# Optimization experiments

Hardware: AMD Instinct MI355X
Metric: run time of the kernel (lower is better)

## Reference

```python
import jax, jax.numpy as jnp
import numpy as np

N = 50000   # nodes
E = 800000  # edges
V = 10000   # vocab
D = 128     # emb_dim
H = 128     # hidden_dim
C = 10      # num_classes
G = 512     # graphs in batch


def setup_inputs() -> dict:
    key = jax.random.key(0)
    ks = jax.random.split(key, 10)
    return {
        "x_tokens": jax.random.randint(ks[0], (N,), 0, V),
        "edge_index": jax.random.randint(ks[1], (2, E), 0, N),
        "batch": jnp.sort(jax.random.randint(ks[2], (N,), 0, G)),
        "emb": jax.random.normal(ks[3], (V, D), dtype=jnp.float32) * 0.05,
        "w1": jax.random.normal(ks[4], (D, H), dtype=jnp.float32) * 0.05,
        "b1": jax.random.normal(ks[5], (H,), dtype=jnp.float32) * 0.05,
        "w2": jax.random.normal(ks[6], (H, H), dtype=jnp.float32) * 0.05,
        "b2": jax.random.normal(ks[7], (H,), dtype=jnp.float32) * 0.05,
        "lin_w": jax.random.normal(ks[8], (H, C), dtype=jnp.float32) * 0.05,
        "lin_b": jax.random.normal(ks[9], (C,), dtype=jnp.float32) * 0.05,
    }


def _gcn_conv(x, W, b, src, dst, norm):
    # PyG GCNConv: x' = D^{-1/2}(A+I)D^{-1/2} X W + b (self-loops already in src/dst)
    h = x @ W                                  # [N, H]
    msg = h[src] * norm[:, None]               # [E+N, H] gather + scale
    return jax.ops.segment_sum(msg, dst, num_segments=N) + b


def reference(x_tokens, edge_index, batch, emb, w1, b1, w2, b2, lin_w, lin_b):
    # embedding with padding_idx=0 (row 0 forced to zero)
    table = emb * (jnp.arange(V) != 0)[:, None].astype(emb.dtype)
    x = table[x_tokens]                        # [N, D]

    # add self loops, symmetric degree normalization (computed once)
    loops = jnp.arange(N)
    src = jnp.concatenate([edge_index[0], loops])
    dst = jnp.concatenate([edge_index[1], loops])
    deg = jax.ops.segment_sum(jnp.ones_like(dst, dtype=x.dtype), dst, num_segments=N)
    dis = jax.lax.rsqrt(deg)                   # deg >= 1 due to self loops
    norm = dis[src] * dis[dst]                 # [E+N]

    x = jax.nn.relu(_gcn_conv(x, w1, b1, src, dst, norm))
    x = jax.nn.relu(_gcn_conv(x, w2, b2, src, dst, norm))

    # global mean pool over graphs
    sums = jax.ops.segment_sum(x, batch, num_segments=G)          # [G, H]
    cnts = jax.ops.segment_sum(jnp.ones((N,), x.dtype), batch, num_segments=G)
    pooled = sums / jnp.maximum(cnts, 1.0)[:, None]

    return pooled @ lin_w + lin_b              # [G, C]
```

## Files before the change

### kernel.cpp

```cpp
#include <hip/hip_runtime.h>
#include <hip/hip_bf16.h>


typedef unsigned int uint;
typedef unsigned short ushort;
typedef __attribute__((ext_vector_type(8))) short bf16x8;
typedef __attribute__((ext_vector_type(4))) float f32x4;

__device__ inline float bf_lo(uint u) { return __uint_as_float(u << 16); }
__device__ inline float bf_hi(uint u) { return __uint_as_float(u & 0xffff0000u); }
__device__ inline ushort f2bf(float f) {
    uint u = __float_as_uint(f);
    return (ushort)((u + 0x7fffu + ((u >> 16) & 1u)) >> 16);
}
__device__ inline uint pack2bf(float a, float b) {
    return (uint)f2bf(a) | ((uint)f2bf(b) << 16);
}

#define EPB 2048
#define CAP 8192

__global__ __launch_bounds__(256) void init_convert(int4* __restrict__ z, int n4,
                                                    const float* __restrict__ W1,
                                                    const float* __restrict__ W2,
                                                    ushort* __restrict__ W1t,
                                                    ushort* __restrict__ W2t) {
    const int zb = (n4 + 255) >> 8;
    if ((int)blockIdx.x < zb) {
        int i = blockIdx.x * 256 + threadIdx.x;
        if (i < n4) z[i] = make_int4(0, 0, 0, 0);
    } else {
        int i = (blockIdx.x - zb) * 256 + threadIdx.x;
        const float* Ws = (i < 16384) ? W1 : W2;
        ushort* Wd      = (i < 16384) ? W1t : W2t;
        int j = i & 16383;
        int nn = j >> 7, k = j & 127;
        Wd[j] = f2bf(Ws[k * 128 + nn]);
    }
}

__global__ __launch_bounds__(256) void bucket_scatter(const int* __restrict__ src,
                                                      const int* __restrict__ dst,
                                                      int* __restrict__ bcur,
                                                      uint* __restrict__ bstage,
                                                      int E, int NB) {
    __shared__ int lh[256];
    __shared__ int lbase[257];
    __shared__ int gbase[256];
    __shared__ int lcur[256];
    __shared__ uint stage[EPB];
    const int t = threadIdx.x;
    const int base = blockIdx.x * EPB;
    const int end  = min(E, base + EPB);
    const int tot  = end - base;

    lh[t] = 0;
    __syncthreads();

    uint pk[8]; int bk[8]; int cnt = 0;
    for (int i = base + t; i < end; i += 256) {
        int s = src[i];
        uint d = (uint)dst[i];
        bk[cnt] = (int)(d >> 8);
        pk[cnt] = (uint)s | ((d & 255u) << 24);
        atomicAdd(&lh[bk[cnt]], 1);
        ++cnt;
    }
    __syncthreads();

    if (t < NB && lh[t]) gbase[t] = t * CAP + atomicAdd(&bcur[t], lh[t]);
    {
        __shared__ int ls[256];
        int v = lh[t];
        ls[t] = v;
        __syncthreads();
        for (int off = 1; off < 256; off <<= 1) {
            int x = (t >= off) ? ls[t - off] : 0;
            __syncthreads();
            ls[t] += x;
            __syncthreads();
        }
        lbase[t] = ls[t] - v;
        if (t == 255) lbase[256] = ls[255];
        lcur[t] = 0;
    }
    __syncthreads();

    for (int j = 0; j < cnt; ++j) {
        int p = lbase[bk[j]] + atomicAdd(&lcur[bk[j]], 1);
        stage[p] = pk[j];
    }
    __syncthreads();

    for (int i = t; i < tot; i += 256) {
        int lo = 0, hi = 256;
        while (lo + 1 < hi) {
            int mid = (lo + hi) >> 1;
            if (lbase[mid] <= i) lo = mid; else hi = mid;
        }
        bstage[gbase[lo] + (i - lbase[lo])] = stage[i];
    }
}

__global__ __launch_bounds__(256) void csr_build(const uint* __restrict__ bstage,
                                                 const int* __restrict__ bcur,
                                                 float* __restrict__ dis,
                                                 int* __restrict__ rbeg,
                                                 int* __restrict__ rend,
                                                 int* __restrict__ csr,
                                                 int N, int NB) {
    __shared__ int lh[256];
    __shared__ int ls[256];
    __shared__ int lbase[256];
    __shared__ int lcur[256];
    const int b = blockIdx.x;
    const int t = threadIdx.x;
    const int base  = b * CAP;
    const int cntb  = bcur[b];
    const int n0    = b << 8;
    const int nn    = min(256, N - n0);

    lh[t] = 0;
    __syncthreads();
    for (int i = t; i < cntb; i += 256)
        atomicAdd(&lh[bstage[base + i] >> 24], 1);
    __syncthreads();

    const int v = lh[t];
    ls[t] = v;
    __syncthreads();
    for (int off = 1; off < 256; off <<= 1) {
        int x = (t >= off) ? ls[t - off] : 0;
        __syncthreads();
        ls[t] += x;
        __syncthreads();
    }
    lbase[t] = ls[t] - v;
    lcur[t] = 0;
    if (t < nn) {
        dis[n0 + t]  = rsqrtf((float)v + 1.0f);
        rbeg[n0 + t] = base + lbase[t];
        rend[n0 + t] = base + lbase[t] + v;
    }
    __syncthreads();

    for (int i = t; i < cntb; i += 256) {
        uint e = bstage[base + i];
        int dl = (int)(e >> 24);
        int pos = base + lbase[dl] + atomicAdd(&lcur[dl], 1);
        csr[pos] = (int)(e & 0xFFFFFFu);
    }
}

template<bool GATHER>
__global__ __launch_bounds__(256) void gemm_mfma(const ushort* __restrict__ Xbf,
                                                 const int* __restrict__ tokens,
                                                 const float* __restrict__ emb,
                                                 const ushort* __restrict__ Wt,
                                                 const float* __restrict__ dis,
                                                 ushort* __restrict__ Out, int n) {
    __shared__ ushort wl[128 * 128];
    const int tid = threadIdx.x;

    {
        const int row  = tid >> 1;
        const int half = tid & 1;
        const int base = row * 256 + half * 128;
#pragma unroll
        for (int i = 0; i < 8; ++i) {
            int off = base + i * 16;
            uint4 v = *(const uint4*)((const char*)Wt + off);
            int swz = off ^ ((row & 7) << 4);
            *(uint4*)((char*)wl + swz) = v;
        }
    }
    __syncthreads();

    const int w  = tid >> 6;
    const int l  = tid & 63;
    const int lr = l & 15;
    const int lg = l >> 4;
    const int rowBase = blockIdx.x * 128 + w * 32;

    f32x4 acc[2][8];
#pragma unroll
    for (int s = 0; s < 2; ++s)
#pragma unroll
        for (int ct = 0; ct < 8; ++ct) acc[s][ct] = (f32x4){0.f, 0.f, 0.f, 0.f};

    bf16x8 afrag[2][4];
#pragma unroll
    for (int s = 0; s < 2; ++s) {
        const int row = rowBase + s * 16 + lr;
        if (row < n) {
            if (GATHER) {
                const int tok = tokens[row];
                if (tok != 0) {
                    const float* ep = emb + (size_t)tok * 128;
#pragma unroll
                    for (int kk = 0; kk < 4; ++kk) {
                        const float* q = ep + kk * 32 + lg * 8;
                        float4 lo = *(const float4*)q;
                        float4 hi = *(const float4*)(q + 4);
                        uint4 pk;
                        pk.x = pack2bf(lo.x, lo.y); pk.y = pack2bf(lo.z, lo.w);
                        pk.z = pack2bf(hi.x, hi.y); pk.w = pack2bf(hi.z, hi.w);
                        union { uint4 u; bf16x8 b; } c; c.u = pk;
                        afrag[s][kk] = c.b;
                    }
                } else {
#pragma unroll
                    for (int kk = 0; kk < 4; ++kk) afrag[s][kk] = (bf16x8){0,0,0,0,0,0,0,0};
                }
            } else {
                const ushort* xp = Xbf + (size_t)row * 128;
#pragma unroll
                for (int kk = 0; kk < 4; ++kk)
                    afrag[s][kk] = *(const bf16x8*)(xp + kk * 32 + lg * 8);
            }
        } else {
#pragma unroll
            for (int kk = 0; kk < 4; ++kk) afrag[s][kk] = (bf16x8){0,0,0,0,0,0,0,0};
        }
    }

#pragma unroll
    for (int ct = 0; ct < 8; ++ct) {
#pragma unroll
        for (int kk = 0; kk < 4; ++kk) {
            const int nrow = ct * 16 + lr;
            int off = nrow * 256 + kk * 64 + lg * 16;
            off ^= ((nrow & 7) << 4);
            bf16x8 b = *(const bf16x8*)((const char*)wl + off);
            acc[0][ct] = __builtin_amdgcn_mfma_f32_16x16x32_bf16(afrag[0][kk], b, acc[0][ct], 0, 0, 0);
            acc[1][ct] = __builtin_amdgcn_mfma_f32_16x16x32_bf16(afrag[1][kk], b, acc[1][ct], 0, 0, 0);
        }
    }

#pragma unroll
    for (int s = 0; s < 2; ++s) {
#pragma unroll
        for (int r = 0; r < 4; ++r) {
            const int row = rowBase + s * 16 + lg * 4 + r;
            if (row < n) {
                const float sc = dis[row];
                ushort* op = Out + (size_t)row * 128 + lr;
#pragma unroll
                for (int ct = 0; ct < 8; ++ct)
                    op[ct * 16] = f2bf(acc[s][ct][r] * sc);
            }
        }
    }
}

template<bool FUSE_POOL>
__global__ __launch_bounds__(256) void aggregate_kernel(const ushort* __restrict__ H,
                                                        const float* __restrict__ dis,
                                                        const int* __restrict__ rbeg,
                                                        const int* __restrict__ rend,
                                                        const int* __restrict__ csr,
                                                        const float* __restrict__ bias,
                                                        ushort* __restrict__ Out,
                                                        const int* __restrict__ batch,
                                                        float* __restrict__ pooled,
                                                        int n) {
    const int g = threadIdx.x >> 4;
    const int l = threadIdx.x & 15;
    const int node = blockIdx.x * 16 + g;
    const bool valid = node < n;

    float s0_=0.f,s1_=0.f,s2_=0.f,s3_=0.f,s4_=0.f,s5_=0.f,s6_=0.f,s7_=0.f;
    float dn = 0.f;
    const float4 bA = *(const float4*)&bias[l * 8];
    const float4 bB = *(const float4*)&bias[l * 8 + 4];

    if (valid) {
        dn = dis[node];
        const uint4 hq = *(const uint4*)(H + (size_t)node * 128 + l * 8);
        s0_ = bf_lo(hq.x); s1_ = bf_hi(hq.x);
        s2_ = bf_lo(hq.y); s3_ = bf_hi(hq.y);
        s4_ = bf_lo(hq.z); s5_ = bf_hi(hq.z);
        s6_ = bf_lo(hq.w); s7_ = bf_hi(hq.w);

        const int e0 = rbeg[node];
        const int e1 = rend[node];
        int e = e0;
        for (; e + 8 <= e1; e += 8) {
            int a[8];
#pragma unroll
            for (int j = 0; j < 8; ++j) a[j] = csr[e + j];
            uint4 h[8];
#pragma unroll
            for (int j = 0; j < 8; ++j) h[j] = *(const uint4*)(H + (size_t)a[j] * 128 + l * 8);
#pragma unroll
            for (int j = 0; j < 8; ++j) {
                s0_ += bf_lo(h[j].x); s1_ += bf_hi(h[j].x);
                s2_ += bf_lo(h[j].y); s3_ += bf_hi(h[j].y);
                s4_ += bf_lo(h[j].z); s5_ += bf_hi(h[j].z);
                s6_ += bf_lo(h[j].w); s7_ += bf_hi(h[j].w);
            }
        }
        for (; e + 4 <= e1; e += 4) {
            int a[4];
#pragma unroll
            for (int j = 0; j < 4; ++j) a[j] = csr[e + j];
            uint4 h[4];
#pragma unroll
            for (int j = 0; j < 4; ++j) h[j] = *(const uint4*)(H + (size_t)a[j] * 128 + l * 8);
#pragma unroll
            for (int j = 0; j < 4; ++j) {
                s0_ += bf_lo(h[j].x); s1_ += bf_hi(h[j].x);
                s2_ += bf_lo(h[j].y); s3_ += bf_hi(h[j].y);
                s4_ += bf_lo(h[j].z); s5_ += bf_hi(h[j].z);
                s6_ += bf_lo(h[j].w); s7_ += bf_hi(h[j].w);
            }
        }
        for (; e < e1; ++e) {
            const uint4 h = *(const uint4*)(H + (size_t)csr[e] * 128 + l * 8);
            s0_ += bf_lo(h.x); s1_ += bf_hi(h.x);
            s2_ += bf_lo(h.y); s3_ += bf_hi(h.y);
            s4_ += bf_lo(h.z); s5_ += bf_hi(h.z);
            s6_ += bf_lo(h.w); s7_ += bf_hi(h.w);
        }
    }

    const float o0 = fmaxf(s0_ * dn + bA.x, 0.0f);
    const float o1 = fmaxf(s1_ * dn + bA.y, 0.0f);
    const float o2 = fmaxf(s2_ * dn + bA.z, 0.0f);
    const float o3 = fmaxf(s3_ * dn + bA.w, 0.0f);
    const float o4 = fmaxf(s4_ * dn + bB.x, 0.0f);
    const float o5 = fmaxf(s5_ * dn + bB.y, 0.0f);
    const float o6 = fmaxf(s6_ * dn + bB.z, 0.0f);
    const float o7 = fmaxf(s7_ * dn + bB.w, 0.0f);

    if constexpr (!FUSE_POOL) {
        if (valid) {
            uint4 o;
            o.x = pack2bf(o0, o1); o.y = pack2bf(o2, o3);
            o.z = pack2bf(o4, o5); o.w = pack2bf(o6, o7);
            *(uint4*)(Out + (size_t)node * 128 + l * 8) = o;
        }
    } else {
        __shared__ float x3[16][128];
        __shared__ int bv[16];
        if (valid) {
            float4 va, vb;
            va.x = o0; va.y = o1; va.z = o2; va.w = o3;
            vb.x = o4; vb.y = o5; vb.z = o6; vb.w = o7;
            *(float4*)&x3[g][l * 8]     = va;
            *(float4*)&x3[g][l * 8 + 4] = vb;
            if (l == 0) bv[g] = batch[node];
        } else if (l == 0) {
            bv[g] = -1;
        }
        __syncthreads();
        const int t = threadIdx.x;
        if (t < 128) {
            int cur = bv[0];
            float run = 0.0f;
            for (int r = 0; r < 16; ++r) {
                const int b = bv[r];
                if (b < 0) break;
                if (b != cur) {
                    if (run != 0.0f) atomicAdd(&pooled[(size_t)cur * 128 + t], run);
                    cur = b; run = 0.0f;
                }
                run += x3[r][t];
            }
            if (cur >= 0 && run != 0.0f) atomicAdd(&pooled[(size_t)cur * 128 + t], run);
        }
    }
}

__global__ __launch_bounds__(128) void pool_finalize(const float* __restrict__ pooled,
                                                     const int* __restrict__ batch,
                                                     const float* __restrict__ lw,
                                                     const float* __restrict__ lb,
                                                     float* __restrict__ out, int n) {
    const int g = blockIdx.x;
    const int t = threadIdx.x;
    int lo = 0, hi = n;
    while (lo < hi) { int mid = (lo + hi) >> 1; if (batch[mid] < g) lo = mid + 1; else hi = mid; }
    const int s = lo;
    hi = n;
    while (lo < hi) { int mid = (lo + hi) >> 1; if (batch[mid] < g + 1) lo = mid + 1; else hi = mid; }
    const float c = fmaxf((float)(lo - s), 1.0f);

    __shared__ float pl[128];
    pl[t] = pooled[(size_t)g * 128 + t] / c;
    __syncthreads();
    if (t < 10) {
        float acc = lb[t];
#pragma unroll 16
        for (int d = 0; d < 128; ++d) acc += pl[d] * lw[d * 10 + t];
        out[g * 10 + t] = acc;
    }
}

extern "C" void kernel_launch(void* const* d_in, const int* in_sizes, int n_in,
                              void* d_out, int out_size, void* d_ws, size_t ws_size,
                              hipStream_t stream) {
    const int*   tokens = (const int*)d_in[0];
    const int*   eidx   = (const int*)d_in[1];
    const int*   batch  = (const int*)d_in[2];
    const float* emb    = (const float*)d_in[3];
    const float* w1     = (const float*)d_in[4];
    const float* b1     = (const float*)d_in[5];
    const float* w2     = (const float*)d_in[6];
    const float* b2     = (const float*)d_in[7];
    const float* lw     = (const float*)d_in[8];
    const float* lbv    = (const float*)d_in[9];

    const int N = in_sizes[0];
    const int E = in_sizes[1] / 2;
    const int G = out_size / 10;
    const int* src = eidx;
    const int* dst = eidx + E;
    const int NB = (N + 255) >> 8;

    char* p = (char*)d_ws;
    auto alloc = [&](size_t bytes) { void* r = (void*)p; p += (bytes + 255) & ~(size_t)255; return r; };
    float*  dis    = (float*)alloc((size_t)N * 4);
    int*    rbeg   = (int*)  alloc((size_t)N * 4);
    int*    rend   = (int*)  alloc((size_t)N * 4);
    int*    zreg   = (int*)  alloc((size_t)(256 + (size_t)G * 128) * 4);
    int*    bcur   = zreg;
    float*  pooled = (float*)(zreg + 256);
    uint*   bstage = (uint*) alloc((size_t)NB * CAP * 4);
    int*    csr    = (int*)  alloc((size_t)NB * CAP * 4);
    ushort* W1t    = (ushort*)alloc(16384 * 2);
    ushort* W2t    = (ushort*)alloc(16384 * 2);
    ushort* A      = (ushort*)alloc((size_t)N * 128 * 2);
    ushort* B      = (ushort*)alloc((size_t)N * 128 * 2);

    const int ZN4 = (256 + G * 128) / 4;
    const int ZB  = (ZN4 + 255) / 256;
    const int EB  = (E + EPB - 1) / EPB;

    init_convert  <<<ZB + 128, 256, 0, stream>>>((int4*)zreg, ZN4, w1, w2, W1t, W2t);
    bucket_scatter<<<EB, 256, 0, stream>>>(src, dst, bcur, bstage, E, NB);
    csr_build     <<<NB, 256, 0, stream>>>(bstage, bcur, dis, rbeg, rend, csr, N, NB);

    gemm_mfma<true><<<(N + 127) / 128, 256, 0, stream>>>(nullptr, tokens, emb, W1t, dis, A, N);
    aggregate_kernel<false><<<(N + 15) / 16, 256, 0, stream>>>(A, dis, rbeg, rend, csr, b1, B, nullptr, nullptr, N);

    gemm_mfma<false><<<(N + 127) / 128, 256, 0, stream>>>(B, nullptr, nullptr, W2t, dis, A, N);
    aggregate_kernel<true><<<(N + 15) / 16, 256, 0, stream>>>(A, dis, rbeg, rend, csr, b2, nullptr, batch, pooled, N);

    pool_finalize<<<G, 128, 0, stream>>>(pooled, batch, lw, lbv, (float*)d_out, N);
}
```

Measured before the change: 142.6 us.

## Merge CSR build with first GEMM by deferring source-degree scaling to aggregation

The first GEMM no longer scales its output by the degree normalisation, so it has no dependency on the CSR build. It now runs in the same launch as csr_build and the pooled-buffer zeroing, which removes one kernel launch and lets the two independent workloads overlap. The first aggregation instead reads dis[src] per edge and applies the self-loop term separately, which adds one extra gathered load per edge. The second layer keeps the pre-scaled path.

Measured after the change: 137.0 us. -4.0%, faster.

```diff
diff --git a/kernel.cpp b/kernel.cpp
--- a/kernel.cpp
+++ b/kernel.cpp
@@ -20,17 +20,15 @@
 #define EPB 2048
 #define CAP 8192
 
-__global__ __launch_bounds__(256) void init_convert(int4* __restrict__ z, int n4,
-                                                    const float* __restrict__ W1,
-                                                    const float* __restrict__ W2,
-                                                    ushort* __restrict__ W1t,
-                                                    ushort* __restrict__ W2t) {
-    const int zb = (n4 + 255) >> 8;
-    if ((int)blockIdx.x < zb) {
-        int i = blockIdx.x * 256 + threadIdx.x;
-        if (i < n4) z[i] = make_int4(0, 0, 0, 0);
+__global__ __launch_bounds__(256) void init0(int* __restrict__ bcur,
+                                             const float* __restrict__ W1,
+                                             const float* __restrict__ W2,
+                                             ushort* __restrict__ W1t,
+                                             ushort* __restrict__ W2t) {
+    if (blockIdx.x == 0) {
+        bcur[threadIdx.x] = 0;
     } else {
-        int i = (blockIdx.x - zb) * 256 + threadIdx.x;
+        int i = (blockIdx.x - 1) * 256 + threadIdx.x;
         const float* Ws = (i < 16384) ? W1 : W2;
         ushort* Wd      = (i < 16384) ? W1t : W2t;
         int j = i & 16383;
@@ -102,18 +100,18 @@
     }
 }
 
-__global__ __launch_bounds__(256) void csr_build(const uint* __restrict__ bstage,
-                                                 const int* __restrict__ bcur,
-                                                 float* __restrict__ dis,
-                                                 int* __restrict__ rbeg,
-                                                 int* __restrict__ rend,
-                                                 int* __restrict__ csr,
-                                                 int N, int NB) {
-    __shared__ int lh[256];
-    __shared__ int ls[256];
-    __shared__ int lbase[256];
-    __shared__ int lcur[256];
-    const int b = blockIdx.x;
+__device__ void csr_body(int* lds,
+                         const uint* __restrict__ bstage,
+                         const int* __restrict__ bcur,
+                         float* __restrict__ dis,
+                         int* __restrict__ rbeg,
+                         int* __restrict__ rend,
+                         int* __restrict__ csr,
+                         int N, int b) {
+    int* lh    = lds;
+    int* ls    = lds + 256;
+    int* lbase = lds + 512;
+    int* lcur  = lds + 768;
     const int t = threadIdx.x;
     const int base  = b * CAP;
     const int cntb  = bcur[b];
@@ -152,16 +150,15 @@
     }
 }
 
-template<bool GATHER>
-__global__ __launch_bounds__(256) void gemm_mfma(const ushort* __restrict__ Xbf,
-                                                 const int* __restrict__ tokens,
-                                                 const float* __restrict__ emb,
-                                                 const ushort* __restrict__ Wt,
-                                                 const float* __restrict__ dis,
-                                                 ushort* __restrict__ Out, int n) {
-    __shared__ ushort wl[128 * 128];
+template<bool GATHER, bool SCALE>
+__device__ void gemm_body(ushort* wl,
+                          const ushort* __restrict__ Xbf,
+                          const int* __restrict__ tokens,
+                          const float* __restrict__ emb,
+                          const ushort* __restrict__ Wt,
+                          const float* __restrict__ dis,
+                          ushort* __restrict__ Out, int n, int bid) {
     const int tid = threadIdx.x;
-
     {
         const int row  = tid >> 1;
         const int half = tid & 1;
@@ -180,7 +177,7 @@
     const int l  = tid & 63;
     const int lr = l & 15;
     const int lg = l >> 4;
-    const int rowBase = blockIdx.x * 128 + w * 32;
+    const int rowBase = bid * 128 + w * 32;
 
     f32x4 acc[2][8];
 #pragma unroll
@@ -243,7 +240,7 @@
         for (int r = 0; r < 4; ++r) {
             const int row = rowBase + s * 16 + lg * 4 + r;
             if (row < n) {
-                const float sc = dis[row];
+                const float sc = SCALE ? dis[row] : 1.0f;
                 ushort* op = Out + (size_t)row * 128 + lr;
 #pragma unroll
                 for (int ct = 0; ct < 8; ++ct)
@@ -253,17 +250,131 @@
     }
 }
 
-template<bool FUSE_POOL>
-__global__ __launch_bounds__(256) void aggregate_kernel(const ushort* __restrict__ H,
-                                                        const float* __restrict__ dis,
-                                                        const int* __restrict__ rbeg,
-                                                        const int* __restrict__ rend,
-                                                        const int* __restrict__ csr,
-                                                        const float* __restrict__ bias,
-                                                        ushort* __restrict__ Out,
-                                                        const int* __restrict__ batch,
-                                                        float* __restrict__ pooled,
-                                                        int n) {
+__global__ __launch_bounds__(256) void csr_gemm1_fused(const uint* __restrict__ bstage,
+                                                       const int* __restrict__ bcur,
+                                                       float* __restrict__ dis,
+                                                       int* __restrict__ rbeg,
+                                                       int* __restrict__ rend,
+                                                       int* __restrict__ csr,
+                                                       const int* __restrict__ tokens,
+                                                       const float* __restrict__ emb,
+                                                       const ushort* __restrict__ W1t,
+                                                       ushort* __restrict__ H,
+                                                       int4* __restrict__ poolz, int pz4,
+                                                       int N, int NB, int GB) {
+    __shared__ ushort wl[128 * 128];
+    const int b = blockIdx.x;
+    if (b < NB) {
+        csr_body((int*)wl, bstage, bcur, dis, rbeg, rend, csr, N, b);
+    } else if (b < NB + GB) {
+        gemm_body<true, false>(wl, nullptr, tokens, emb, W1t, nullptr, H, N, b - NB);
+    } else {
+        int i = (b - NB - GB) * 256 + threadIdx.x;
+        if (i < pz4) poolz[i] = make_int4(0, 0, 0, 0);
+    }
+}
+
+__global__ __launch_bounds__(256) void gemm2_kernel(const ushort* __restrict__ Xbf,
+                                                    const ushort* __restrict__ Wt,
+                                                    const float* __restrict__ dis,
+                                                    ushort* __restrict__ Out, int n) {
+    __shared__ ushort wl[128 * 128];
+    gemm_body<false, true>(wl, Xbf, nullptr, nullptr, Wt, dis, Out, n, blockIdx.x);
+}
+
+__global__ __launch_bounds__(256) void aggregate_w(const ushort* __restrict__ H,
+                                                   const float* __restrict__ dis,
+                                                   const int* __restrict__ rbeg,
+                                                   const int* __restrict__ rend,
+                                                   const int* __restrict__ csr,
+                                                   const float* __restrict__ bias,
+                                                   ushort* __restrict__ Out, int n) {
+    const int g = threadIdx.x >> 4;
+    const int l = threadIdx.x & 15;
+    const int node = blockIdx.x * 16 + g;
+    if (node >= n) return;
+
+    const float dn = dis[node];
+    const uint4 hq = *(const uint4*)(H + (size_t)node * 128 + l * 8);
+    const int e0 = rbeg[node];
+    const int e1 = rend[node];
+
+    float s0_=0.f,s1_=0.f,s2_=0.f,s3_=0.f,s4_=0.f,s5_=0.f,s6_=0.f,s7_=0.f;
+
+    int e = e0;
+    for (; e + 8 <= e1; e += 8) {
+        int a[8];
+#pragma unroll
+        for (int j = 0; j < 8; ++j) a[j] = csr[e + j];
+        float w[8];
+#pragma unroll
+        for (int j = 0; j < 8; ++j) w[j] = dis[a[j]];
+        uint4 h[8];
+#pragma unroll
+        for (int j = 0; j < 8; ++j) h[j] = *(const uint4*)(H + (size_t)a[j] * 128 + l * 8);
+#pragma unroll
+        for (int j = 0; j < 8; ++j) {
+            s0_ += bf_lo(h[j].x) * w[j]; s1_ += bf_hi(h[j].x) * w[j];
+            s2_ += bf_lo(h[j].y) * w[j]; s3_ += bf_hi(h[j].y) * w[j];
+            s4_ += bf_lo(h[j].z) * w[j]; s5_ += bf_hi(h[j].z) * w[j];
+            s6_ += bf_lo(h[j].w) * w[j]; s7_ += bf_hi(h[j].w) * w[j];
+        }
+    }
+    for (; e + 4 <= e1; e += 4) {
+        int a[4];
+#pragma unroll
+        for (int j = 0; j < 4; ++j) a[j] = csr[e + j];
+        float w[4];
+#pragma unroll
+        for (int j = 0; j < 4; ++j) w[j] = dis[a[j]];
+        uint4 h[4];
+#pragma unroll
+        for (int j = 0; j < 4; ++j) h[j] = *(const uint4*)(H + (size_t)a[j] * 128 + l * 8);
+#pragma unroll
+        for (int j = 0; j < 4; ++j) {
+            s0_ += bf_lo(h[j].x) * w[j]; s1_ += bf_hi(h[j].x) * w[j];
+            s2_ += bf_lo(h[j].y) * w[j]; s3_ += bf_hi(h[j].y) * w[j];
+            s4_ += bf_lo(h[j].z) * w[j]; s5_ += bf_hi(h[j].z) * w[j];
+            s6_ += bf_lo(h[j].w) * w[j]; s7_ += bf_hi(h[j].w) * w[j];
+        }
+    }
+    for (; e < e1; ++e) {
+        const int a = csr[e];
+        const float w = dis[a];
+        const uint4 h = *(const uint4*)(H + (size_t)a * 128 + l * 8);
+        s0_ += bf_lo(h.x)*w; s1_ += bf_hi(h.x)*w;
+        s2_ += bf_lo(h.y)*w; s3_ += bf_hi(h.y)*w;
+        s4_ += bf_lo(h.z)*w; s5_ += bf_hi(h.z)*w;
+        s6_ += bf_lo(h.w)*w; s7_ += bf_hi(h.w)*w;
+    }
+
+    const float self = dn * dn;
+    const float4 bA = *(const float4*)&bias[l * 8];
+    const float4 bB = *(const float4*)&bias[l * 8 + 4];
+    float o0 = fmaxf(s0_ * dn + bf_lo(hq.x) * self + bA.x, 0.0f);
+    float o1 = fmaxf(s1_ * dn + bf_hi(hq.x) * self + bA.y, 0.0f);
+    float o2 = fmaxf(s2_ * dn + bf_lo(hq.y) * self + bA.z, 0.0f);
+    float o3 = fmaxf(s3_ * dn + bf_hi(hq.y) * self + bA.w, 0.0f);
+    float o4 = fmaxf(s4_ * dn + bf_lo(hq.z) * self + bB.x, 0.0f);
+    float o5 = fmaxf(s5_ * dn + bf_hi(hq.z) * self + bB.y, 0.0f);
+    float o6 = fmaxf(s6_ * dn + bf_lo(hq.w) * self + bB.z, 0.0f);
+    float o7 = fmaxf(s7_ * dn + bf_hi(hq.w) * self + bB.w, 0.0f);
+
+    uint4 o;
+    o.x = pack2bf(o0, o1); o.y = pack2bf(o2, o3);
+    o.z = pack2bf(o4, o5); o.w = pack2bf(o6, o7);
+    *(uint4*)(Out + (size_t)node * 128 + l * 8) = o;
+}
+
+__global__ __launch_bounds__(256) void aggregate_pool(const ushort* __restrict__ H,
+                                                      const float* __restrict__ dis,
+                                                      const int* __restrict__ rbeg,
+                                                      const int* __restrict__ rend,
+                                                      const int* __restrict__ csr,
+                                                      const float* __restrict__ bias,
+                                                      const int* __restrict__ batch,
+                                                      float* __restrict__ pooled,
+                                                      int n) {
     const int g = threadIdx.x >> 4;
     const int l = threadIdx.x & 15;
     const int node = blockIdx.x * 16 + g;
@@ -333,42 +444,33 @@
     const float o6 = fmaxf(s6_ * dn + bB.z, 0.0f);
     const float o7 = fmaxf(s7_ * dn + bB.w, 0.0f);
 
-    if constexpr (!FUSE_POOL) {
-        if (valid) {
-            uint4 o;
-            o.x = pack2bf(o0, o1); o.y = pack2bf(o2, o3);
-            o.z = pack2bf(o4, o5); o.w = pack2bf(o6, o7);
-            *(uint4*)(Out + (size_t)node * 128 + l * 8) = o;
-        }
-    } else {
-        __shared__ float x3[16][128];
-        __shared__ int bv[16];
-        if (valid) {
-            float4 va, vb;
-            va.x = o0; va.y = o1; va.z = o2; va.w = o3;
-            vb.x = o4; vb.y = o5; vb.z = o6; vb.w = o7;
-            *(float4*)&x3[g][l * 8]     = va;
-            *(float4*)&x3[g][l * 8 + 4] = vb;
-            if (l == 0) bv[g] = batch[node];
-        } else if (l == 0) {
-            bv[g] = -1;
-        }
-        __syncthreads();
-        const int t = threadIdx.x;
-        if (t < 128) {
-            int cur = bv[0];
-            float run = 0.0f;
-            for (int r = 0; r < 16; ++r) {
-                const int b = bv[r];
-                if (b < 0) break;
-                if (b != cur) {
-                    if (run != 0.0f) atomicAdd(&pooled[(size_t)cur * 128 + t], run);
-                    cur = b; run = 0.0f;
-                }
-                run += x3[r][t];
+    __shared__ float x3[16][128];
+    __shared__ int bv[16];
+    if (valid) {
+        float4 va, vb;
+        va.x = o0; va.y = o1; va.z = o2; va.w = o3;
+        vb.x = o4; vb.y = o5; vb.z = o6; vb.w = o7;
+        *(float4*)&x3[g][l * 8]     = va;
+        *(float4*)&x3[g][l * 8 + 4] = vb;
+        if (l == 0) bv[g] = batch[node];
+    } else if (l == 0) {
+        bv[g] = -1;
+    }
+    __syncthreads();
+    const int t = threadIdx.x;
+    if (t < 128) {
+        int cur = bv[0];
+        float run = 0.0f;
+        for (int r = 0; r < 16; ++r) {
+            const int b = bv[r];
+            if (b < 0) break;
+            if (b != cur) {
+                if (run != 0.0f) atomicAdd(&pooled[(size_t)cur * 128 + t], run);
+                cur = b; run = 0.0f;
             }
-            if (cur >= 0 && run != 0.0f) atomicAdd(&pooled[(size_t)cur * 128 + t], run);
-        }
+            run += x3[r][t];
+        }
+        if (cur >= 0 && run != 0.0f) atomicAdd(&pooled[(size_t)cur * 128 + t], run);
     }
 }
 
@@ -417,15 +519,15 @@
     const int* src = eidx;
     const int* dst = eidx + E;
     const int NB = (N + 255) >> 8;
+    const int GB = (N + 127) / 128;
 
     char* p = (char*)d_ws;
     auto alloc = [&](size_t bytes) { void* r = (void*)p; p += (bytes + 255) & ~(size_t)255; return r; };
     float*  dis    = (float*)alloc((size_t)N * 4);
     int*    rbeg   = (int*)  alloc((size_t)N * 4);
     int*    rend   = (int*)  alloc((size_t)N * 4);
-    int*    zreg   = (int*)  alloc((size_t)(256 + (size_t)G * 128) * 4);
-    int*    bcur   = zreg;
-    float*  pooled = (float*)(zreg + 256);
+    int*    bcur   = (int*)  alloc(256 * 4);
+    float*  pooled = (float*)alloc((size_t)G * 128 * 4);
     uint*   bstage = (uint*) alloc((size_t)NB * CAP * 4);
     int*    csr    = (int*)  alloc((size_t)NB * CAP * 4);
     ushort* W1t    = (ushort*)alloc(16384 * 2);
@@ -433,19 +535,17 @@
     ushort* A      = (ushort*)alloc((size_t)N * 128 * 2);
     ushort* B      = (ushort*)alloc((size_t)N * 128 * 2);
 
-    const int ZN4 = (256 + G * 128) / 4;
-    const int ZB  = (ZN4 + 255) / 256;
+    const int PZ4 = (G * 128) / 4;
+    const int PZB = (PZ4 + 255) / 256;
     const int EB  = (E + EPB - 1) / EPB;
 
-    init_convert  <<<ZB + 128, 256, 0, stream>>>((int4*)zreg, ZN4, w1, w2, W1t, W2t);
+    init0<<<129, 256, 0, stream>>>(bcur, w1, w2, W1t, W2t);
     bucket_scatter<<<EB, 256, 0, stream>>>(src, dst, bcur, bstage, E, NB);
-    csr_build     <<<NB, 256, 0, stream>>>(bstage, bcur, dis, rbeg, rend, csr, N, NB);
-
-    gemm_mfma<true><<<(N + 127) / 128, 256, 0, stream>>>(nullptr, tokens, emb, W1t, dis, A, N);
-    aggregate_kernel<false><<<(N + 15) / 16, 256, 0, stream>>>(A, dis, rbeg, rend, csr, b1, B, nullptr, nullptr, N);
-
-    gemm_mfma<false><<<(N + 127) / 128, 256, 0, stream>>>(B, nullptr, nullptr, W2t, dis, A, N);
-    aggregate_kernel<true><<<(N + 15) / 16, 256, 0, stream>>>(A, dis, rbeg, rend, csr, b2, nullptr, batch, pooled, N);
-
+    csr_gemm1_fused<<<NB + GB + PZB, 256, 0, stream>>>(bstage, bcur, dis, rbeg, rend, csr,
+                                                       tokens, emb, W1t, A,
+                                                       (int4*)pooled, PZ4, N, NB, GB);
+    aggregate_w<<<(N + 15) / 16, 256, 0, stream>>>(A, dis, rbeg, rend, csr, b1, B, N);
+    gemm2_kernel<<<GB, 256, 0, stream>>>(B, W2t, dis, A, N);
+    aggregate_pool<<<(N + 15) / 16, 256, 0, stream>>>(A, dis, rbeg, rend, csr, b2, batch, pooled, N);
     pool_finalize<<<G, 128, 0, stream>>>(pooled, batch, lw, lbv, (float*)d_out, N);
 }
```
